# Performance work log

Hardware: AMD Instinct MI355X
Metric: run time of the kernel (lower is better)

## Reference

```python
import jax, jax.numpy as jnp
import numpy as np

B, TF, TE = 64, 64, 32
FV, EV = 30000, 20000
E, H = 40, 100
SP = 256


def _gru(h, x, W, U, b):
    # Keras GRU cell (reset_after=True): W [in,3H], U [H,3H], b [2,3H]
    xs = x @ W + b[0]
    hs = h @ U + b[1]
    xz, xr, xh = jnp.split(xs, 3, axis=-1)
    hz, hr, hh = jnp.split(hs, 3, axis=-1)
    z = jax.nn.sigmoid(xz + hz)
    r = jax.nn.sigmoid(xr + hr)
    cand = jnp.tanh(xh + r * hh)
    return z * h + (1.0 - z) * cand


def setup_inputs() -> dict:
    key = jax.random.key(0)
    ks = jax.random.split(key, 16)
    p = lambda i, shape, s=0.01: jax.random.normal(ks[i], shape, jnp.float32) * s
    return {
        "encoder_input": jax.random.randint(ks[0], (B, TF), 0, FV),
        "decoder_input": jax.random.randint(ks[1], (B, TE), 0, EV),
        "french_embed": p(2, (FV, E)),
        "eng_embed": p(3, (EV, E)),
        "enc_W": p(4, (E, 3 * H), 0.1), "enc_U": p(5, (H, 3 * H), 0.1), "enc_b": jnp.zeros((2, 3 * H), jnp.float32),
        "dec_W": p(6, (H, 3 * H), 0.1), "dec_U": p(7, (H, 3 * H), 0.1), "dec_b": jnp.zeros((2, 3 * H), jnp.float32),
        "att_W1": p(8, (2 * H, 2 * H)), "att_W2": p(9, (H, 2 * H)),
        "sp1_W": p(10, (3 * H, SP), 0.1), "sp1_b": jnp.zeros((SP,), jnp.float32),
        "sp2_W": p(11, (SP, SP), 0.1), "sp2_b": jnp.zeros((SP,), jnp.float32),
        "ff1_W": p(12, (H, H), 0.1), "ff1_b": jnp.zeros((H,), jnp.float32),
        "ff2_W": p(13, (H, EV), 0.1), "ff2_b": jnp.zeros((EV,), jnp.float32),
    }


def reference(encoder_input, decoder_input, french_embed, eng_embed,
              enc_W, enc_U, enc_b, dec_W, dec_U, dec_b,
              att_W1, att_W2, sp1_W, sp1_b, sp2_W, sp2_b,
              ff1_W, ff1_b, ff2_W, ff2_b):
    b = encoder_input.shape[0]
    x = french_embed[encoder_input]            # [B,TF,E]
    _ = eng_embed[decoder_input]               # embedded in original call() but never consumed

    # ---- encoder GRU over french sequence ----
    def enc_step(h, xt):
        h2 = _gru(h, xt, enc_W, enc_U, enc_b)
        return h2, h2
    h0 = jnp.zeros((b, H), x.dtype)
    enc_state, enc_seq = jax.lax.scan(enc_step, h0, jnp.swapaxes(x, 0, 1))
    enc_outputs = jnp.swapaxes(enc_seq, 0, 1)  # [B,TF,H]

    # ---- decoder: per-step additive attention + GRU + scratchpad enc_output rewrite ----
    def dec_step(carry, _):
        h, enc = carry
        hb = jnp.broadcast_to(h[:, None, :], enc.shape)
        keys = jnp.tanh(jnp.concatenate([hb, enc], axis=-1) @ att_W1)   # [B,TF,2H]
        query = h @ att_W2                                               # [B,2H]
        scores = jnp.einsum('btd,bd->bt', keys, query)
        alpha = jax.nn.softmax(scores, axis=-1)
        read = jnp.einsum('bt,bth->bh', alpha, enc)                      # attentive read [B,H]
        h_new = _gru(h, read, dec_W, dec_U, dec_b)
        # scratchpad: per-position write gate, rewrite enc towards attentive read
        z = jnp.concatenate([
            jnp.broadcast_to(h_new[:, None, :], enc.shape),
            jnp.broadcast_to(read[:, None, :], enc.shape),
            enc], axis=-1)                                               # [B,TF,3H]
        g = jax.nn.sigmoid(jnp.mean(jax.nn.relu(z @ sp1_W + sp1_b) @ sp2_W + sp2_b,
                                    axis=-1, keepdims=True))             # [B,TF,1]
        enc_new = g * enc + (1.0 - g) * read[:, None, :]
        return (h_new, enc_new), h_new

    n_steps = decoder_input.shape[1]
    (_, _), dec_seq = jax.lax.scan(dec_step, (enc_state, enc_outputs), None, length=n_steps)
    dec_out = jnp.swapaxes(dec_seq, 0, 1)      # [B,TE,H]

    hid = jax.nn.relu(dec_out @ ff1_W + ff1_b)
    probs = jax.nn.softmax(hid @ ff2_W + ff2_b, axis=-1)  # [B,TE,EV]
    return probs
```

## Files before the change

kernel.cpp:

```cpp
#include <hip/hip_runtime.h>
#include <math.h>

#define B 64
#define TF 64
#define TE 32
#define E_DIM 40
#define H 100
#define H2 200
#define H3 300
#define SP 256
#define EV 20000
#define ROWS (B*TF)
#define NC 1012

__global__ __launch_bounds__(256) void k_setup(const float* att_W1, const float* dec_W,
        const float* sp1_W, const float* sp2_W, const float* sp2_b,
        float* W_all, float* v, float* c2) {
  int bid = blockIdx.x;
  if (bid < 396) {
    int idx = bid*256 + threadIdx.x;
    if (idx < 100*NC) {
      int k = idx / NC, c = idx - k*NC;
      float val;
      if (c < 200)      val = att_W1[(100+k)*H2 + c];
      else if (c < 456) val = sp1_W[(200+k)*SP + (c-200)];
      else if (c < 756) val = dec_W[k*H3 + (c-456)];
      else              val = sp1_W[(100+k)*SP + (c-756)];
      W_all[idx] = val;
    }
  } else if (bid == 396) {
    int k = threadIdx.x;
    float s = 0.f;
    for (int j = 0; j < SP; ++j) s += sp2_W[k*SP + j];
    v[k] = s * (1.f/256.f);
  } else {
    if (threadIdx.x == 0) {
      float s = 0.f;
      for (int j = 0; j < SP; ++j) s += sp2_b[j];
      *c2 = s * (1.f/256.f);
    }
  }
}

__global__ __launch_bounds__(320) void k_embed(const int* enc_in, const float* femb,
        const float* enc_W, const float* enc_b, float* xs_all) {
  int row = blockIdx.x;
  int j = threadIdx.x;
  __shared__ __align__(16) float emb[E_DIM];
  int tok = enc_in[row];
  if (j < E_DIM) emb[j] = femb[tok*E_DIM + j];
  __syncthreads();
  if (j < H3) {
    float acc = enc_b[j];
    #pragma unroll
    for (int k = 0; k < E_DIM; ++k) acc += emb[k]*enc_W[k*H3 + j];
    xs_all[row*H3 + j] = acc;
  }
}

__global__ __launch_bounds__(192) void k_enc(const float* __restrict__ enc_U,
        const float* __restrict__ enc_b, const float* __restrict__ xs_all,
        float* __restrict__ enc_T, float* __restrict__ h_state) {
  int b = blockIdx.x, t = threadIdx.x;
  __shared__ __align__(16) float hsh[104];
  __shared__ __align__(16) float hs[304];

  float2 Ur[100];
  float2 bias = {0.f, 0.f};
  if (t < 150) {
    const float* base = enc_U + 2*t;
    #pragma unroll
    for (int k = 0; k < 100; ++k) Ur[k] = *(const float2*)(base + k*H3);
    bias = *(const float2*)(enc_b + H3 + 2*t);
  }
  if (t < H) hsh[t] = 0.f;
  __syncthreads();

  #pragma unroll 1
  for (int step = 0; step < TF; ++step) {
    int row = b*TF + step;
    float xz = 0.f, xr = 0.f, xh = 0.f;
    if (t < H) {
      xz = xs_all[row*H3 + t];
      xr = xs_all[row*H3 + 100 + t];
      xh = xs_all[row*H3 + 200 + t];
    }
    if (t < 150) {
      float a0 = bias.x, a1 = bias.y;
      const float4* h4 = (const float4*)hsh;
      #pragma unroll
      for (int k4 = 0; k4 < 25; ++k4) {
        float4 hv = h4[k4];
        a0 += hv.x*Ur[k4*4+0].x + hv.y*Ur[k4*4+1].x + hv.z*Ur[k4*4+2].x + hv.w*Ur[k4*4+3].x;
        a1 += hv.x*Ur[k4*4+0].y + hv.y*Ur[k4*4+1].y + hv.z*Ur[k4*4+2].y + hv.w*Ur[k4*4+3].y;
      }
      hs[2*t]   = a0;
      hs[2*t+1] = a1;
    }
    __syncthreads();
    if (t < H) {
      float z = 1.f/(1.f+expf(-(xz + hs[t])));
      float r = 1.f/(1.f+expf(-(xr + hs[100+t])));
      float cand = tanhf(xh + r*hs[200+t]);
      float hn = z*hsh[t] + (1.f-z)*cand;
      hsh[t] = hn;
      enc_T[t*ROWS + row] = hn;
    }
    __syncthreads();
  }
  if (t < H) h_state[b*H + t] = hsh[t];
}

#define KC 20
__global__ __launch_bounds__(256) void k_initQ(const float* __restrict__ enc_T,
        const float* __restrict__ W_all, float* __restrict__ Q_g) {
  int bx = blockIdx.x, by = blockIdx.y;
  int tid = threadIdx.x;
  int tx = tid & 15, ty = tid >> 4;
  __shared__ __align__(16) float At[KC*132];
  __shared__ __align__(16) float Wt[KC*132];
  int r0 = by*128;
  int c0 = bx*128;
  float acc[8][8];
  #pragma unroll
  for (int i = 0; i < 8; ++i)
    #pragma unroll
    for (int j = 0; j < 8; ++j) acc[i][j] = 0.f;
  for (int kc = 0; kc < 100; kc += KC) {
    __syncthreads();
    for (int i = tid; i < 128*KC; i += 256) {
      int r = i & 127, kk = i >> 7;
      At[kk*132 + r] = enc_T[(kc+kk)*ROWS + r0 + r];
    }
    for (int i = tid; i < 128*KC; i += 256) {
      int cidx = i & 127, kk = i >> 7;
      int gc = c0 + cidx;
      Wt[kk*132 + cidx] = (gc < NC) ? W_all[(kc+kk)*NC + gc] : 0.f;
    }
    __syncthreads();
    #pragma unroll
    for (int kk = 0; kk < KC; ++kk) {
      const float* Ar = At + kk*132;
      const float* Wr = Wt + kk*132;
      float4 a0 = *(const float4*)(Ar + ty*4);
      float4 a1 = *(const float4*)(Ar + 64 + ty*4);
      float4 w0 = *(const float4*)(Wr + tx*4);
      float4 w1 = *(const float4*)(Wr + 64 + tx*4);
      float av[8] = {a0.x,a0.y,a0.z,a0.w,a1.x,a1.y,a1.z,a1.w};
      float wv[8] = {w0.x,w0.y,w0.z,w0.w,w1.x,w1.y,w1.z,w1.w};
      #pragma unroll
      for (int i = 0; i < 8; ++i)
        #pragma unroll
        for (int j = 0; j < 8; ++j) acc[i][j] += av[i]*wv[j];
    }
  }
  #pragma unroll
  for (int i = 0; i < 8; ++i) {
    int r = r0 + ty*4 + (i < 4 ? i : 60 + i);
    float* orow = Q_g + (size_t)r*NC;
    int ca = c0 + tx*4;
    if (ca < NC) {
      float4 val = {acc[i][0], acc[i][1], acc[i][2], acc[i][3]};
      *(float4*)(orow + ca) = val;
    }
    int cb = c0 + 64 + tx*4;
    if (cb < NC) {
      float4 val = {acc[i][4], acc[i][5], acc[i][6], acc[i][7]};
      *(float4*)(orow + cb) = val;
    }
  }
}

__global__ __launch_bounds__(512, 1) void k_dec(
    const float* __restrict__ Q_g, const float* __restrict__ h_st,
    const float* __restrict__ dec_U, const float* __restrict__ dec_b,
    const float* __restrict__ sp1_W, const float* __restrict__ sp1_b,
    const float* __restrict__ att_W1, const float* __restrict__ att_W2,
    const float* __restrict__ v_g, const float* __restrict__ c2p,
    float* __restrict__ dec_o) {
  int b = blockIdx.x, tid = threadIdx.x;
  int w = tid >> 6, lane = tid & 63;
  __shared__ float Psc[64*200];
  __shared__ float PYs[64*256];
  __shared__ __align__(16) float Rsh[1016];
  __shared__ __align__(16) float hL[104];
  __shared__ float hWs[200], qs[200], ccs[256], vL[256], spb[256];
  __shared__ __align__(16) float dbs[600];
  __shared__ float xsx[304], hsx[304];
  __shared__ __align__(16) float scor[64];
  __shared__ __align__(16) float alph[64];
  __shared__ __align__(16) float gsh[64];

  float qd[64];
  float qm[64];

  const float* Qb = Q_g + (size_t)b*64*NC;

  for (int i = tid; i < 12800; i += 512) {
    int t = i / 200, c = i - t*200;
    Psc[i] = Qb[t*NC + c];
  }
  for (int i = tid; i < 16384; i += 512) {
    int t = i >> 8, j = i & 255;
    PYs[i] = Qb[t*NC + 200 + j];
  }
  if (tid < 300) {
    #pragma unroll
    for (int t = 0; t < 64; ++t) qd[t] = Qb[t*NC + 456 + tid];
  }
  if (tid < 256) {
    #pragma unroll
    for (int t = 0; t < 64; ++t) qm[t] = Qb[t*NC + 756 + tid];
    vL[tid] = v_g[tid];
    spb[tid] = sp1_b[tid];
  }
  if (tid < 104) hL[tid] = (tid < 100) ? h_st[b*100 + tid] : 0.f;
  for (int i = tid; i < 600; i += 512) dbs[i] = dec_b[i];
  float c2 = *c2p;
  __syncthreads();
  for (int cx = tid; cx < 400; cx += 512) {
    const float* Wm = (cx < 200) ? att_W1 : att_W2;
    int col = (cx < 200) ? cx : cx - 200;
    float a = 0.f;
    #pragma unroll 5
    for (int k = 0; k < 100; ++k) a += hL[k]*Wm[k*H2 + col];
    if (cx < 200) hWs[col] = a; else qs[col] = a;
  }
  __syncthreads();

  #pragma unroll 1
  for (int s = 0; s < TE; ++s) {
    #pragma unroll
    for (int i = 0; i < 8; ++i) {
      int t = w*8 + i;
      float sp = 0.f;
      for (int c = lane; c < 200; c += 64)
        sp += tanhf(hWs[c] + Psc[t*200 + c]) * qs[c];
      #pragma unroll
      for (int mk = 32; mk >= 1; mk >>= 1) sp += __shfl_xor(sp, mk);
      if (lane == 0) scor[t] = sp;
    }
    __syncthreads();
    if (w == 0) {
      float sc = scor[lane];
      float m = sc;
      #pragma unroll
      for (int mk = 32; mk >= 1; mk >>= 1) m = fmaxf(m, __shfl_xor(m, mk));
      float ex = expf(sc - m);
      float ssum = ex;
      #pragma unroll
      for (int mk = 32; mk >= 1; mk >>= 1) ssum += __shfl_xor(ssum, mk);
      alph[lane] = ex / ssum;
    }
    __syncthreads();
    if (tid < 300) {
      float r = 0.f;
      #pragma unroll
      for (int t4 = 0; t4 < 16; ++t4) {
        float4 a4 = *(const float4*)(alph + t4*4);
        r += a4.x*qd[t4*4+0] + a4.y*qd[t4*4+1] + a4.z*qd[t4*4+2] + a4.w*qd[t4*4+3];
      }
      Rsh[456 + tid] = r;
    }
    if (tid < 256) {
      float r = 0.f;
      #pragma unroll
      for (int t4 = 0; t4 < 16; ++t4) {
        float4 a4 = *(const float4*)(alph + t4*4);
        r += a4.x*qm[t4*4+0] + a4.y*qm[t4*4+1] + a4.z*qm[t4*4+2] + a4.w*qm[t4*4+3];
      }
      Rsh[756 + tid] = r;
      float rp = 0.f;
      #pragma unroll 8
      for (int t = 0; t < 64; ++t) rp += alph[t]*PYs[t*256 + tid];
      Rsh[200 + tid] = rp;
    } else if (tid >= 300 && tid < 500) {
      int c = tid - 300;
      float rs = 0.f;
      #pragma unroll 8
      for (int t = 0; t < 64; ++t) rs += alph[t]*Psc[t*200 + c];
      Rsh[c] = rs;
    }
    __syncthreads();
    if (tid < 300) {
      float a = dbs[300 + tid];
      #pragma unroll 5
      for (int k = 0; k < 100; ++k) a += hL[k]*dec_U[k*H3 + tid];
      hsx[tid] = a;
      xsx[tid] = Rsh[456 + tid] + dbs[tid];
    }
    __syncthreads();
    if (tid < 100) {
      float xz = xsx[tid], xr = xsx[100+tid], xh = xsx[200+tid];
      float hz = hsx[tid], hr = hsx[100+tid], hh = hsx[200+tid];
      float hv = hL[tid];
      float z = 1.f/(1.f+expf(-(xz+hz)));
      float r = 1.f/(1.f+expf(-(xr+hr)));
      float cand = tanhf(xh + r*hh);
      float hn = z*hv + (1.f-z)*cand;
      hL[tid] = hn;
      dec_o[(b*TE + s)*H + tid] = hn;
    }
    __syncthreads();
    for (int cx = tid; cx < 656; cx += 512) {
      if (cx < 256) {
        float a = 0.f;
        #pragma unroll 5
        for (int k = 0; k < 100; ++k) a += hL[k]*sp1_W[k*SP + cx];
        ccs[cx] = a + Rsh[756 + cx] + spb[cx];
      } else {
        int cy = cx - 256;
        const float* Wm = (cy < 200) ? att_W1 : att_W2;
        int col = (cy < 200) ? cy : cy - 200;
        float a = 0.f;
        #pragma unroll 5
        for (int k = 0; k < 100; ++k) a += hL[k]*Wm[k*H2 + col];
        if (cy < 200) hWs[col] = a; else qs[col] = a;
      }
    }
    __syncthreads();
    #pragma unroll
    for (int i = 0; i < 8; ++i) {
      int t = w*8 + i;
      float gp = 0.f;
      #pragma unroll
      for (int jj = 0; jj < 4; ++jj) {
        int j = lane + jj*64;
        gp += fmaxf(ccs[j] + PYs[t*256 + j], 0.f) * vL[j];
      }
      #pragma unroll
      for (int mk = 32; mk >= 1; mk >>= 1) gp += __shfl_xor(gp, mk);
      if (lane == 0) gsh[t] = 1.f/(1.f+expf(-(gp + c2)));
    }
    __syncthreads();
    for (int i = tid; i < 12800; i += 512) {
      int t = i / 200, c = i - t*200;
      float g = gsh[t];
      Psc[i] = g*Psc[i] + (1.f-g)*Rsh[c];
    }
    for (int i = tid; i < 16384; i += 512) {
      int t = i >> 8, j = i & 255;
      float g = gsh[t];
      PYs[i] = g*PYs[i] + (1.f-g)*Rsh[200 + j];
    }
    if (tid < 300) {
      float rv = Rsh[456 + tid];
      #pragma unroll
      for (int t4 = 0; t4 < 16; ++t4) {
        float4 g4 = *(const float4*)(gsh + t4*4);
        qd[t4*4+0] = g4.x*qd[t4*4+0] + (1.f-g4.x)*rv;
        qd[t4*4+1] = g4.y*qd[t4*4+1] + (1.f-g4.y)*rv;
        qd[t4*4+2] = g4.z*qd[t4*4+2] + (1.f-g4.z)*rv;
        qd[t4*4+3] = g4.w*qd[t4*4+3] + (1.f-g4.w)*rv;
      }
    }
    if (tid < 256) {
      float rv = Rsh[756 + tid];
      #pragma unroll
      for (int t4 = 0; t4 < 16; ++t4) {
        float4 g4 = *(const float4*)(gsh + t4*4);
        qm[t4*4+0] = g4.x*qm[t4*4+0] + (1.f-g4.x)*rv;
        qm[t4*4+1] = g4.y*qm[t4*4+1] + (1.f-g4.y)*rv;
        qm[t4*4+2] = g4.z*qm[t4*4+2] + (1.f-g4.z)*rv;
        qm[t4*4+3] = g4.w*qm[t4*4+3] + (1.f-g4.w)*rv;
      }
    }
    __syncthreads();
  }
}

__global__ __launch_bounds__(128) void k_ff1(const float* dec_out, const float* ff1_W,
        const float* ff1_b, float* hid) {
  int row = blockIdx.x, j = threadIdx.x;
  __shared__ __align__(16) float a[104];
  if (j < H) a[j] = dec_out[row*H + j];
  __syncthreads();
  if (j < H) {
    float acc = ff1_b[j];
    const float4* a4 = (const float4*)a;
    #pragma unroll
    for (int k4 = 0; k4 < 25; ++k4) {
      float4 av = a4[k4];
      int k = k4*4;
      acc += av.x*ff1_W[(k+0)*H+j] + av.y*ff1_W[(k+1)*H+j] + av.z*ff1_W[(k+2)*H+j] + av.w*ff1_W[(k+3)*H+j];
    }
    hid[row*H + j] = fmaxf(acc, 0.f);
  }
}

__global__ __launch_bounds__(256) void k_logits(const float* hid, const float* ff2_W,
        const float* ff2_b, float* out) {
  int bx = blockIdx.x, by = blockIdx.y;
  int tid = threadIdx.x;
  int tx = tid & 15, ty = tid >> 4;
  __shared__ __align__(16) float At[KC*132];
  __shared__ __align__(16) float Wt[KC*132];
  int r0 = by*128;
  int c0 = bx*128;
  float acc[8][8];
  #pragma unroll
  for (int i = 0; i < 8; ++i) {
    #pragma unroll
    for (int j = 0; j < 8; ++j) acc[i][j] = 0.f;
  }
  for (int kc = 0; kc < 100; kc += KC) {
    __syncthreads();
    for (int i = tid; i < 128*KC; i += 256) {
      int r = i & 127, kk = i >> 7;
      At[kk*132 + r] = hid[(r0+r)*H + kc + kk];
    }
    for (int i = tid; i < 128*KC; i += 256) {
      int cidx = i & 127, kk = i >> 7;
      int gc = c0 + cidx;
      Wt[kk*132 + cidx] = (gc < EV) ? ff2_W[(size_t)(kc+kk)*EV + gc] : 0.f;
    }
    __syncthreads();
    #pragma unroll
    for (int kk = 0; kk < KC; ++kk) {
      const float* Ar = At + kk*132;
      const float* Wr = Wt + kk*132;
      float4 a0 = *(const float4*)(Ar + ty*4);
      float4 a1 = *(const float4*)(Ar + 64 + ty*4);
      float4 w0 = *(const float4*)(Wr + tx*4);
      float4 w1 = *(const float4*)(Wr + 64 + tx*4);
      float av[8] = {a0.x,a0.y,a0.z,a0.w,a1.x,a1.y,a1.z,a1.w};
      float wv[8] = {w0.x,w0.y,w0.z,w0.w,w1.x,w1.y,w1.z,w1.w};
      #pragma unroll
      for (int i = 0; i < 8; ++i) {
        #pragma unroll
        for (int j = 0; j < 8; ++j) acc[i][j] += av[i]*wv[j];
      }
    }
  }
  #pragma unroll
  for (int i = 0; i < 8; ++i) {
    int r = r0 + ty*4 + (i < 4 ? i : 60 + i);
    float* orow = out + (size_t)r*EV;
    int ca = c0 + tx*4;
    if (ca < EV) {
      float4 bb = *(const float4*)(ff2_b + ca);
      float4 val = {acc[i][0]+bb.x, acc[i][1]+bb.y, acc[i][2]+bb.z, acc[i][3]+bb.w};
      *(float4*)(orow + ca) = val;
    }
    int cb = c0 + 64 + tx*4;
    if (cb < EV) {
      float4 bb = *(const float4*)(ff2_b + cb);
      float4 val = {acc[i][4]+bb.x, acc[i][5]+bb.y, acc[i][6]+bb.z, acc[i][7]+bb.w};
      *(float4*)(orow + cb) = val;
    }
  }
}

__global__ __launch_bounds__(256) void k_softmax(float* out) {
  int row = blockIdx.x, tid = threadIdx.x;
  float* p = out + (size_t)row*EV;
  float m = -1e30f, ssum = 0.f;
  for (int j = tid; j < EV; j += 256) {
    float x = p[j];
    if (x > m) { ssum = ssum*expf(m - x) + 1.f; m = x; }
    else ssum += expf(x - m);
  }
  __shared__ float sm[256], ss[256];
  sm[tid] = m; ss[tid] = ssum;
  __syncthreads();
  for (int st = 128; st >= 1; st >>= 1) {
    if (tid < st) {
      float m2 = sm[tid+st], s2 = ss[tid+st];
      float M = fmaxf(sm[tid], m2);
      ss[tid] = ss[tid]*expf(sm[tid]-M) + s2*expf(m2-M);
      sm[tid] = M;
    }
    __syncthreads();
  }
  float M = sm[0];
  float inv = 1.f/ss[0];
  for (int j = tid; j < EV; j += 256) {
    p[j] = expf(p[j] - M) * inv;
  }
}

extern "C" void kernel_launch(void* const* d_in, const int* in_sizes, int n_in,
                              void* d_out, int out_size, void* d_ws, size_t ws_size,
                              hipStream_t stream) {
  (void)in_sizes; (void)n_in; (void)out_size;
  const int*   enc_in  = (const int*)d_in[0];
  const float* femb    = (const float*)d_in[2];
  const float* enc_W   = (const float*)d_in[4];
  const float* enc_U   = (const float*)d_in[5];
  const float* enc_b   = (const float*)d_in[6];
  const float* dec_W   = (const float*)d_in[7];
  const float* dec_U   = (const float*)d_in[8];
  const float* dec_b   = (const float*)d_in[9];
  const float* att_W1  = (const float*)d_in[10];
  const float* att_W2  = (const float*)d_in[11];
  const float* sp1_W   = (const float*)d_in[12];
  const float* sp1_b   = (const float*)d_in[13];
  const float* sp2_W   = (const float*)d_in[14];
  const float* sp2_b   = (const float*)d_in[15];
  const float* ff1_W   = (const float*)d_in[16];
  const float* ff1_b   = (const float*)d_in[17];
  const float* ff2_W   = (const float*)d_in[18];
  const float* ff2_b   = (const float*)d_in[19];
  float* out = (float*)d_out;
  float* ws  = (float*)d_ws;

  float* enc_T  = ws + 0;
  float* W_all  = ws + 409600;
  float* h_st   = ws + 510800;
  float* dec_o  = ws + 517200;
  float* hid    = ws + 722000;
  float* vbuf   = ws + 926800;
  float* c2buf  = ws + 927056;
  float* Q_g    = ws + 927072;
  float* xs_all = Q_g;
  if (ws_size < (size_t)5072224*4) return;

  k_setup<<<398, 256, 0, stream>>>(att_W1, dec_W, sp1_W, sp2_W, sp2_b, W_all, vbuf, c2buf);
  k_embed<<<4096, 320, 0, stream>>>(enc_in, femb, enc_W, enc_b, xs_all);
  k_enc<<<64, 192, 0, stream>>>(enc_U, enc_b, xs_all, enc_T, h_st);
  k_initQ<<<dim3(8, 32), 256, 0, stream>>>(enc_T, W_all, Q_g);
  k_dec<<<64, 512, 0, stream>>>(Q_g, h_st, dec_U, dec_b, sp1_W, sp1_b,
                                att_W1, att_W2, vbuf, c2buf, dec_o);
  k_ff1<<<2048, 128, 0, stream>>>(dec_o, ff1_W, ff1_b, hid);
  k_logits<<<dim3(157, 16), 256, 0, stream>>>(hid, ff2_W, ff2_b, out);
  k_softmax<<<2048, 256, 0, stream>>>(out);
}
```

Measured before the change: 1.452 ms.

## Rebalance decoder Q-column state across threads with register float4s and LDS tail

Each of the 512 threads now owns one Q column in 16 float4 registers, replacing the two 64-float register arrays held by the first 300 and first 256 threads, so thread roles no longer overlap and register pressure per thread drops. The leftover 44 columns (968..1011) go to a new shared-memory array that idle threads reduce and blend. The attentive-read work is also redistributed so more threads run the reduction loops in parallel. This aims to reduce per-thread serial work and register spills in the sequential decoder loop, at the cost of extra LDS and an added blend loop.

```diff
diff --git a/kernel.cpp b/kernel.cpp
--- a/kernel.cpp
+++ b/kernel.cpp
@@ -171,6 +171,8 @@
   }
 }
 
+#define Q16(OP) OP(0) OP(1) OP(2) OP(3) OP(4) OP(5) OP(6) OP(7) \
+                OP(8) OP(9) OP(10) OP(11) OP(12) OP(13) OP(14) OP(15)
 __global__ __launch_bounds__(512, 1) void k_dec(
     const float* __restrict__ Q_g, const float* __restrict__ h_st,
     const float* __restrict__ dec_U, const float* __restrict__ dec_b,
@@ -182,6 +184,7 @@
   int w = tid >> 6, lane = tid & 63;
   __shared__ float Psc[64*200];
   __shared__ float PYs[64*256];
+  __shared__ float Qex[64*44];
   __shared__ __align__(16) float Rsh[1016];
   __shared__ __align__(16) float hL[104];
   __shared__ float hWs[200], qs[200], ccs[256], vL[256], spb[256];
@@ -191,11 +194,15 @@
   __shared__ __align__(16) float alph[64];
   __shared__ __align__(16) float gsh[64];
 
-  float qd[64];
-  float qm[64];
-
+  int mycol = (tid < 300) ? (456 + tid) : (756 + (tid - 300));
   const float* Qb = Q_g + (size_t)b*64*NC;
 
+#define DECLQ(i) float4 q##i;
+  Q16(DECLQ)
+
+#define LOADQ(i) q##i = make_float4(Qb[(4*i+0)*NC + mycol], Qb[(4*i+1)*NC + mycol], \
+                                    Qb[(4*i+2)*NC + mycol], Qb[(4*i+3)*NC + mycol]);
+  Q16(LOADQ)
   for (int i = tid; i < 12800; i += 512) {
     int t = i / 200, c = i - t*200;
     Psc[i] = Qb[t*NC + c];
@@ -204,16 +211,11 @@
     int t = i >> 8, j = i & 255;
     PYs[i] = Qb[t*NC + 200 + j];
   }
-  if (tid < 300) {
-    #pragma unroll
-    for (int t = 0; t < 64; ++t) qd[t] = Qb[t*NC + 456 + tid];
-  }
-  if (tid < 256) {
-    #pragma unroll
-    for (int t = 0; t < 64; ++t) qm[t] = Qb[t*NC + 756 + tid];
-    vL[tid] = v_g[tid];
-    spb[tid] = sp1_b[tid];
-  }
+  for (int i = tid; i < 2816; i += 512) {
+    int t = i / 44, e = i - t*44;
+    Qex[i] = Qb[t*NC + 968 + e];
+  }
+  if (tid < 256) { vL[tid] = v_g[tid]; spb[tid] = sp1_b[tid]; }
   if (tid < 104) hL[tid] = (tid < 100) ? h_st[b*100 + tid] : 0.f;
   for (int i = tid; i < 600; i += 512) dbs[i] = dec_b[i];
   float c2 = *c2p;
@@ -253,33 +255,30 @@
       alph[lane] = ex / ssum;
     }
     __syncthreads();
-    if (tid < 300) {
-      float r = 0.f;
-      #pragma unroll
-      for (int t4 = 0; t4 < 16; ++t4) {
-        float4 a4 = *(const float4*)(alph + t4*4);
-        r += a4.x*qd[t4*4+0] + a4.y*qd[t4*4+1] + a4.z*qd[t4*4+2] + a4.w*qd[t4*4+3];
-      }
-      Rsh[456 + tid] = r;
-    }
-    if (tid < 256) {
-      float r = 0.f;
-      #pragma unroll
-      for (int t4 = 0; t4 < 16; ++t4) {
-        float4 a4 = *(const float4*)(alph + t4*4);
-        r += a4.x*qm[t4*4+0] + a4.y*qm[t4*4+1] + a4.z*qm[t4*4+2] + a4.w*qm[t4*4+3];
-      }
-      Rsh[756 + tid] = r;
+    {
+      float rr = 0.f;
+#define REDQ(i) rr += alph[4*i+0]*q##i.x + alph[4*i+1]*q##i.y \
+                    + alph[4*i+2]*q##i.z + alph[4*i+3]*q##i.w;
+      Q16(REDQ)
+      Rsh[mycol] = rr;
+    }
+    if (tid < 200) {
+      float rs = 0.f;
+      #pragma unroll 8
+      for (int t = 0; t < 64; ++t) rs += alph[t]*Psc[t*200 + tid];
+      Rsh[tid] = rs;
+    } else if (tid < 456) {
+      int j = tid - 200;
       float rp = 0.f;
       #pragma unroll 8
-      for (int t = 0; t < 64; ++t) rp += alph[t]*PYs[t*256 + tid];
-      Rsh[200 + tid] = rp;
-    } else if (tid >= 300 && tid < 500) {
-      int c = tid - 300;
-      float rs = 0.f;
+      for (int t = 0; t < 64; ++t) rp += alph[t]*PYs[t*256 + j];
+      Rsh[tid] = rp;
+    } else if (tid < 500) {
+      int e = tid - 456;
+      float re = 0.f;
       #pragma unroll 8
-      for (int t = 0; t < 64; ++t) rs += alph[t]*Psc[t*200 + c];
-      Rsh[c] = rs;
+      for (int t = 0; t < 64; ++t) re += alph[t]*Qex[t*44 + e];
+      Rsh[968 + e] = re;
     }
     __syncthreads();
     if (tid < 300) {
@@ -333,6 +332,13 @@
       if (lane == 0) gsh[t] = 1.f/(1.f+expf(-(gp + c2)));
     }
     __syncthreads();
+    {
+      float rv = Rsh[mycol];
+#define BLDQ(i) { float g0 = gsh[4*i+0], g1 = gsh[4*i+1], g2 = gsh[4*i+2], g3 = gsh[4*i+3]; \
+      q##i.x = g0*q##i.x + (1.f-g0)*rv;  q##i.y = g1*q##i.y + (1.f-g1)*rv; \
+      q##i.z = g2*q##i.z + (1.f-g2)*rv;  q##i.w = g3*q##i.w + (1.f-g3)*rv; }
+      Q16(BLDQ)
+    }
     for (int i = tid; i < 12800; i += 512) {
       int t = i / 200, c = i - t*200;
       float g = gsh[t];
@@ -343,27 +349,10 @@
       float g = gsh[t];
       PYs[i] = g*PYs[i] + (1.f-g)*Rsh[200 + j];
     }
-    if (tid < 300) {
-      float rv = Rsh[456 + tid];
-      #pragma unroll
-      for (int t4 = 0; t4 < 16; ++t4) {
-        float4 g4 = *(const float4*)(gsh + t4*4);
-        qd[t4*4+0] = g4.x*qd[t4*4+0] + (1.f-g4.x)*rv;
-        qd[t4*4+1] = g4.y*qd[t4*4+1] + (1.f-g4.y)*rv;
-        qd[t4*4+2] = g4.z*qd[t4*4+2] + (1.f-g4.z)*rv;
-        qd[t4*4+3] = g4.w*qd[t4*4+3] + (1.f-g4.w)*rv;
-      }
-    }
-    if (tid < 256) {
-      float rv = Rsh[756 + tid];
-      #pragma unroll
-      for (int t4 = 0; t4 < 16; ++t4) {
-        float4 g4 = *(const float4*)(gsh + t4*4);
-        qm[t4*4+0] = g4.x*qm[t4*4+0] + (1.f-g4.x)*rv;
-        qm[t4*4+1] = g4.y*qm[t4*4+1] + (1.f-g4.y)*rv;
-        qm[t4*4+2] = g4.z*qm[t4*4+2] + (1.f-g4.z)*rv;
-        qm[t4*4+3] = g4.w*qm[t4*4+3] + (1.f-g4.w)*rv;
-      }
+    for (int i = tid; i < 2816; i += 512) {
+      int t = i / 44, e = i - t*44;
+      float g = gsh[t];
+      Qex[i] = g*Qex[i] + (1.f-g)*Rsh[968 + e];
     }
     __syncthreads();
   }
```

Result: faster. 1.303 ms (-10.3%).
